# Performance work log

Measured on AMD Instinct MI355X. Metric: run time of the kernel, lower is better.

The kernel has to match this reference:

```python
import jax, jax.numpy as jnp
import numpy as np

D = 128
N = 768
EPS = 1e-5

def _layernorm(x, w, b):
    m = jnp.mean(x, axis=-1, keepdims=True)
    v = jnp.mean(jnp.square(x - m), axis=-1, keepdims=True)
    return (x - m) * jax.lax.rsqrt(v + EPS) * w + b

def _linear(x, w, b):
    # torch Linear convention: w is [out, in]
    return jnp.einsum('...i,oi->...o', x, w) + b

def setup_inputs() -> dict:
    key = jax.random.key(0)
    ks = jax.random.split(key, 8)
    s = 1.0 / np.sqrt(D)
    d = {
        'pair': jax.random.normal(ks[0], (N, N, D), dtype=jnp.float32),
        'ln_in_w': jnp.ones((D,), jnp.float32), 'ln_in_b': jnp.zeros((D,), jnp.float32),
        'lp_w': jax.random.uniform(ks[1], (D, D), jnp.float32, -s, s), 'lp_b': jnp.zeros((D,), jnp.float32),
        'lg_w': jax.random.uniform(ks[2], (D, D), jnp.float32, -s, s), 'lg_b': jnp.zeros((D,), jnp.float32),
        'rp_w': jax.random.uniform(ks[3], (D, D), jnp.float32, -s, s), 'rp_b': jnp.zeros((D,), jnp.float32),
        'rg_w': jax.random.uniform(ks[4], (D, D), jnp.float32, -s, s), 'rg_b': jnp.zeros((D,), jnp.float32),
        'cn_w': jnp.ones((D,), jnp.float32), 'cn_b': jnp.zeros((D,), jnp.float32),
        'op_w': jax.random.uniform(ks[5], (D, D), jnp.float32, -s, s), 'op_b': jnp.zeros((D,), jnp.float32),
        'og_w': jax.random.uniform(ks[6], (D, D), jnp.float32, -s, s), 'og_b': jnp.zeros((D,), jnp.float32),
        'ln_out_w': jnp.ones((D,), jnp.float32), 'ln_out_b': jnp.zeros((D,), jnp.float32),
    }
    return d

def reference(pair, ln_in_w, ln_in_b, lp_w, lp_b, lg_w, lg_b, rp_w, rp_b, rg_w, rg_b,
              cn_w, cn_b, op_w, op_b, og_w, og_b, ln_out_w, ln_out_b):
    z = _layernorm(pair, ln_in_w, ln_in_b)
    left = jax.nn.sigmoid(_linear(z, lg_w, lg_b)) * _linear(z, lp_w, lp_b)
    right = jax.nn.sigmoid(_linear(z, rg_w, rg_b)) * _linear(z, rp_w, rp_b)
    # outgoing direction: pair(i,j) = sum_k left(i,k,d) * right(j,k,d)
    tri = jnp.einsum('ikd,jkd->ijd', left, right)
    tri = _layernorm(tri, cn_w, cn_b)
    tri = jax.nn.sigmoid(_linear(pair, og_w, og_b)) * _linear(tri, op_w, op_b)
    return _layernorm(pair + tri, ln_out_w, ln_out_b)
```

## Files before the change

kernel.cpp:

```cpp
#include <hip/hip_runtime.h>

#define N 768
#define D 128
#define NSQ (N*N)
#define EPS 1e-5f

typedef __bf16 bf16;
typedef __bf16 bf16x8 __attribute__((ext_vector_type(8)));
typedef float f32x4 __attribute__((ext_vector_type(4)));

__device__ __forceinline__ void gld16(const void* g, void* l) {
    __builtin_amdgcn_global_load_lds(
        (const __attribute__((address_space(1))) unsigned int*)g,
        (__attribute__((address_space(3))) unsigned int*)l, 16, 0, 0);
}

__global__ void k_convert_w(const float* __restrict__ lp, const float* __restrict__ lg,
                            const float* __restrict__ rp, const float* __restrict__ rg,
                            const float* __restrict__ op, const float* __restrict__ og,
                            bf16* __restrict__ dst) {
    const float* srcs[6] = {lp, lg, rp, rg, op, og};
    int m = blockIdx.y;
    int i = blockIdx.x * 256 + threadIdx.x;
    dst[m * 16384 + i] = (bf16)srcs[m][i];
}

__global__ __launch_bounds__(512, 2) void k_ln_gate2(
    const float* __restrict__ pair, const float* __restrict__ lnw, const float* __restrict__ lnb,
    const bf16* __restrict__ wbf,
    const float* __restrict__ lp_b, const float* __restrict__ lg_b,
    const float* __restrict__ rp_b, const float* __restrict__ rg_b,
    bf16* __restrict__ left_t, bf16* __restrict__ right_t)
{
    __shared__ bf16 zt[2][64 * 128];

    const int t = threadIdx.x;
    const int lane = t & 63, wid = t >> 6;
    const int side = wid >> 2, dq = wid & 3;
    const int lr = lane & 15, lh = lane >> 4;

    const bf16* wPsrc = wbf + (side ? 2 : 0) * 16384;
    const bf16* wGsrc = wbf + (side ? 3 : 1) * 16384;
    const float* bPp = side ? rp_b : lp_b;
    const float* bGp = side ? rg_b : lg_b;
    bf16* dst = side ? right_t : left_t;

    bf16x8 aP[4][2], aG[4][2];
    #pragma unroll
    for (int kk = 0; kk < 4; ++kk)
        #pragma unroll
        for (int m = 0; m < 2; ++m) {
            int rd = dq * 32 + m * 16 + lr;
            aP[kk][m] = *(const bf16x8*)(wPsrc + rd * 128 + (kk * 4 + lh) * 8);
            aG[kk][m] = *(const bf16x8*)(wGsrc + rd * 128 + (kk * 4 + lh) * 8);
        }

    const int r8 = t >> 3, q = t & 7;

    f32x4 lw0 = *(const f32x4*)(lnw + q * 16);
    f32x4 lw1 = *(const f32x4*)(lnw + q * 16 + 4);
    f32x4 lw2 = *(const f32x4*)(lnw + q * 16 + 8);
    f32x4 lw3 = *(const f32x4*)(lnw + q * 16 + 12);
    f32x4 lb0 = *(const f32x4*)(lnb + q * 16);
    f32x4 lb1 = *(const f32x4*)(lnb + q * 16 + 4);
    f32x4 lb2 = *(const f32x4*)(lnb + q * 16 + 8);
    f32x4 lb3 = *(const f32x4*)(lnb + q * 16 + 12);

    const int bid = blockIdx.x, gstride = gridDim.x;

    f32x4 p0, p1, p2, p3;
    {
        const float* prow = pair + (size_t)(bid * 64 + r8) * 128 + q * 16;
        p0 = *(const f32x4*)(prow);
        p1 = *(const f32x4*)(prow + 4);
        p2 = *(const f32x4*)(prow + 8);
        p3 = *(const f32x4*)(prow + 12);
    }

    int buf = 0;
    for (int tile = bid; tile < NSQ / 64; tile += gstride) {
        const int row0 = tile * 64;

        float x[16];
        #pragma unroll
        for (int e = 0; e < 4; ++e) {
            x[e] = p0[e]; x[4 + e] = p1[e]; x[8 + e] = p2[e]; x[12 + e] = p3[e];
        }
        float s1 = 0.f, s2 = 0.f;
        #pragma unroll
        for (int j = 0; j < 16; ++j) { s1 += x[j]; s2 += x[j] * x[j]; }
        s1 += __shfl_xor(s1, 1); s2 += __shfl_xor(s2, 1);
        s1 += __shfl_xor(s1, 2); s2 += __shfl_xor(s2, 2);
        s1 += __shfl_xor(s1, 4); s2 += __shfl_xor(s2, 4);
        float mean = s1 * (1.f / 128.f);
        float rstd = rsqrtf(s2 * (1.f / 128.f) - mean * mean + EPS);

        bf16x8 pk0, pk1;
        #pragma unroll
        for (int e = 0; e < 4; ++e) {
            pk0[e]     = (bf16)((x[e]      - mean) * rstd * lw0[e] + lb0[e]);
            pk0[4 + e] = (bf16)((x[4 + e]  - mean) * rstd * lw1[e] + lb1[e]);
            pk1[e]     = (bf16)((x[8 + e]  - mean) * rstd * lw2[e] + lb2[e]);
            pk1[4 + e] = (bf16)((x[12 + e] - mean) * rstd * lw3[e] + lb3[e]);
        }
        {
            char* zb = (char*)&zt[buf][0];
            *(bf16x8*)(zb + r8 * 256 + ((q * 2)     ^ (r8 & 7)) * 16) = pk0;
            *(bf16x8*)(zb + r8 * 256 + ((q * 2 + 1) ^ (r8 & 7)) * 16) = pk1;
        }
        __syncthreads();

        int nt = tile + gstride;
        if (nt < NSQ / 64) {
            const float* prow = pair + (size_t)(nt * 64 + r8) * 128 + q * 16;
            p0 = *(const f32x4*)(prow);
            p1 = *(const f32x4*)(prow + 4);
            p2 = *(const f32x4*)(prow + 8);
            p3 = *(const f32x4*)(prow + 12);
        }

        f32x4 accP[2][4] = {};
        f32x4 accG[2][4] = {};
        const char* zb = (const char*)&zt[buf][0];
        #pragma unroll
        for (int kk = 0; kk < 4; ++kk) {
            bf16x8 bz[4];
            #pragma unroll
            for (int n = 0; n < 4; ++n) {
                int rz = n * 16 + lr;
                bz[n] = *(const bf16x8*)(zb + rz * 256 + (((kk * 4 + lh)) ^ (rz & 7)) * 16);
            }
            #pragma unroll
            for (int m = 0; m < 2; ++m)
                #pragma unroll
                for (int n = 0; n < 4; ++n) {
                    accP[m][n] = __builtin_amdgcn_mfma_f32_16x16x32_bf16(aP[kk][m], bz[n], accP[m][n], 0, 0, 0);
                    accG[m][n] = __builtin_amdgcn_mfma_f32_16x16x32_bf16(aG[kk][m], bz[n], accG[m][n], 0, 0, 0);
                }
        }

        #pragma unroll
        for (int m = 0; m < 2; ++m) {
            f32x4 vbP = *(const f32x4*)(bPp + dq * 32 + m * 16 + lh * 4);
            f32x4 vbG = *(const f32x4*)(bGp + dq * 32 + m * 16 + lh * 4);
            #pragma unroll
            for (int reg = 0; reg < 4; ++reg) {
                int d = dq * 32 + m * 16 + lh * 4 + reg;
                #pragma unroll
                for (int n = 0; n < 4; ++n) {
                    float g = accG[m][n][reg] + vbG[reg];
                    float p = accP[m][n][reg] + vbP[reg];
                    float val = p * (1.f / (1.f + __expf(-g)));
                    dst[(size_t)d * NSQ + row0 + n * 16 + lr] = (bf16)val;
                }
            }
        }
        buf ^= 1;
        __syncthreads();
    }
}

__global__ __launch_bounds__(256, 4) void k_tri(
    const bf16* __restrict__ left_t, const bf16* __restrict__ right_t, bf16* __restrict__ tri_t)
{
    __shared__ bf16 at[2][128 * 32];
    __shared__ bf16 bt[2][128 * 32];
    const int t = threadIdx.x;
    const int b = blockIdx.x;
    const int xcd = b & 7;
    const int s = b >> 3;
    const int d = xcd * 16 + s / 36;
    const int tile = s % 36;
    const int ti = tile / 6, tj = tile % 6;
    const bf16* A = left_t + (size_t)d * NSQ;
    const bf16* B = right_t + (size_t)d * NSQ;
    const int i0 = ti * 128, j0 = tj * 128;

    auto stage = [&](int buf, int kt) {
        int k0 = kt * 32;
        #pragma unroll
        for (int c = 0; c < 2; ++c) {
            int sl = c * 256 + t;
            int r = sl >> 2, cp = sl & 3, cl = cp ^ ((r >> 1) & 3);
            gld16(A + (size_t)(i0 + r) * 768 + k0 + cl * 8, (char*)at[buf] + sl * 16);
            gld16(B + (size_t)(j0 + r) * 768 + k0 + cl * 8, (char*)bt[buf] + sl * 16);
        }
    };

    const int lane = t & 63, wid = t >> 6;
    const int wr = wid >> 1, wc = wid & 1;
    const int lr = lane & 15, lh = lane >> 4;

    f32x4 acc[4][4] = {};

    stage(0, 0);
    __syncthreads();
    for (int kt = 0; kt < 24; ++kt) {
        if (kt < 23) stage((kt + 1) & 1, kt + 1);
        const bf16* ab = at[kt & 1];
        const bf16* bb = bt[kt & 1];
        bf16x8 af[4], bff[4];
        #pragma unroll
        for (int m = 0; m < 4; ++m) {
            int r = wr * 64 + m * 16 + lr;
            int phys = lh ^ ((r >> 1) & 3);
            af[m] = *(const bf16x8*)((const char*)ab + r * 64 + phys * 16);
        }
        #pragma unroll
        for (int n = 0; n < 4; ++n) {
            int r = wc * 64 + n * 16 + lr;
            int phys = lh ^ ((r >> 1) & 3);
            bff[n] = *(const bf16x8*)((const char*)bb + r * 64 + phys * 16);
        }
        #pragma unroll
        for (int m = 0; m < 4; ++m)
            #pragma unroll
            for (int n = 0; n < 4; ++n)
                acc[m][n] = __builtin_amdgcn_mfma_f32_16x16x32_bf16(af[m], bff[n], acc[m][n], 0, 0, 0);
        __syncthreads();
    }

    bf16* C = tri_t + (size_t)d * NSQ;
    #pragma unroll
    for (int m = 0; m < 4; ++m)
        #pragma unroll
        for (int n = 0; n < 4; ++n)
            #pragma unroll
            for (int reg = 0; reg < 4; ++reg) {
                int ri = i0 + wr * 64 + m * 16 + lh * 4 + reg;
                int cj = j0 + wc * 64 + n * 16 + lr;
                C[(size_t)ri * 768 + cj] = (bf16)acc[m][n][reg];
            }
}

__global__ __launch_bounds__(256, 2) void k_cln(
    const bf16* __restrict__ tri_t, const float* __restrict__ cnw, const float* __restrict__ cnb,
    bf16* __restrict__ tri_ln)
{
    __shared__ bf16 tile[256 * 128];
    __shared__ float mrs[256][2];
    const int t = threadIdx.x;
    const size_t ij = (size_t)blockIdx.x * 256 + t;
    float s1 = 0.f, s2 = 0.f;
    for (int dc = 0; dc < 16; ++dc) {
        bf16x8 pk;
        #pragma unroll
        for (int e = 0; e < 8; ++e) {
            int dd = dc * 8 + e;
            bf16 raw = tri_t[(size_t)dd * NSQ + ij];
            float v = (float)raw;
            s1 += v; s2 += v * v;
            pk[e] = raw;
        }
        *(bf16x8*)((char*)tile + t * 256 + (dc ^ (t & 7)) * 16) = pk;
    }
    float mean = s1 * (1.f / 128.f);
    float rstd = rsqrtf(s2 * (1.f / 128.f) - mean * mean + EPS);
    mrs[t][0] = mean; mrs[t][1] = rstd;
    __syncthreads();
    const size_t ij0 = (size_t)blockIdx.x * 256;
    #pragma unroll
    for (int c = 0; c < 16; ++c) {
        int sl = c * 256 + t;
        int rl = sl >> 4, cp = sl & 15, cl = cp ^ (rl & 7);
        bf16x8 raw = *(const bf16x8*)((const char*)tile + rl * 256 + cp * 16);
        float m = mrs[rl][0], r = mrs[rl][1];
        f32x4 w0 = *(const f32x4*)(cnw + cl * 8);
        f32x4 w1 = *(const f32x4*)(cnw + cl * 8 + 4);
        f32x4 b0 = *(const f32x4*)(cnb + cl * 8);
        f32x4 b1 = *(const f32x4*)(cnb + cl * 8 + 4);
        bf16x8 o;
        #pragma unroll
        for (int e = 0; e < 4; ++e) {
            o[e]     = (bf16)(((float)raw[e]     - m) * r * w0[e] + b0[e]);
            o[4 + e] = (bf16)(((float)raw[4 + e] - m) * r * w1[e] + b1[e]);
        }
        *(bf16x8*)(tri_ln + (ij0 + rl) * 128 + cl * 8) = o;
    }
}

__global__ __launch_bounds__(512, 2) void k_final2(
    const float* __restrict__ pair, const bf16* __restrict__ tri_ln,
    const bf16* __restrict__ wbf,
    const float* __restrict__ op_b, const float* __restrict__ og_b,
    const float* __restrict__ lnow, const float* __restrict__ lnob,
    float* __restrict__ out)
{
    __shared__ bf16 zt[64 * 128];
    __shared__ bf16 tt[2][64 * 128];
    __shared__ float ub[64 * 132];

    const int t = threadIdx.x;
    const int lane = t & 63, wid = t >> 6;
    const int dq = wid & 3, wh = wid >> 2;
    const int lr = lane & 15, lh = lane >> 4;

    const bf16* opsrc = wbf + 4 * 16384;
    const bf16* ogsrc = wbf + 5 * 16384;

    bf16x8 aOG[4][2], aOP[4][2];
    #pragma unroll
    for (int kk = 0; kk < 4; ++kk)
        #pragma unroll
        for (int m = 0; m < 2; ++m) {
            int rd = dq * 32 + m * 16 + lr;
            aOG[kk][m] = *(const bf16x8*)(ogsrc + rd * 128 + (kk * 4 + lh) * 8);
            aOP[kk][m] = *(const bf16x8*)(opsrc + rd * 128 + (kk * 4 + lh) * 8);
        }
    f32x4 vbOG[2], vbOP[2];
    #pragma unroll
    for (int m = 0; m < 2; ++m) {
        vbOG[m] = *(const f32x4*)(og_b + dq * 32 + m * 16 + lh * 4);
        vbOP[m] = *(const f32x4*)(op_b + dq * 32 + m * 16 + lh * 4);
    }

    const int r8 = t >> 3, q = t & 7;
    f32x4 lw0 = *(const f32x4*)(lnow + q * 16);
    f32x4 lw1 = *(const f32x4*)(lnow + q * 16 + 4);
    f32x4 lw2 = *(const f32x4*)(lnow + q * 16 + 8);
    f32x4 lw3 = *(const f32x4*)(lnow + q * 16 + 12);
    f32x4 lb0 = *(const f32x4*)(lnob + q * 16);
    f32x4 lb1 = *(const f32x4*)(lnob + q * 16 + 4);
    f32x4 lb2 = *(const f32x4*)(lnob + q * 16 + 8);
    f32x4 lb3 = *(const f32x4*)(lnob + q * 16 + 12);

    const int bid = blockIdx.x, gstride = gridDim.x;

    auto stage_tt = [&](int buf, int tile) {
        const int row0 = tile * 64;
        #pragma unroll
        for (int c = 0; c < 2; ++c) {
            int s = c * 512 + t;
            int r = s >> 4, cp = s & 15, cl = cp ^ (r & 7);
            gld16(tri_ln + (size_t)(row0 + r) * 128 + cl * 8, (char*)tt[buf] + s * 16);
        }
    };

    f32x4 pA0, pA1, pA2, pA3;
    {
        const float* prow = pair + (size_t)(bid * 64 + r8) * 128 + q * 16;
        pA0 = *(const f32x4*)(prow);
        pA1 = *(const f32x4*)(prow + 4);
        pA2 = *(const f32x4*)(prow + 8);
        pA3 = *(const f32x4*)(prow + 12);
    }
    stage_tt(0, bid);

    int buf = 0;
    for (int tile = bid; tile < NSQ / 64; tile += gstride) {
        const int row0 = tile * 64;

        {
            bf16x8 pk0, pk1;
            #pragma unroll
            for (int e = 0; e < 4; ++e) {
                pk0[e]     = (bf16)pA0[e];
                pk0[4 + e] = (bf16)pA1[e];
                pk1[e]     = (bf16)pA2[e];
                pk1[4 + e] = (bf16)pA3[e];
            }
            char* zb = (char*)zt;
            *(bf16x8*)(zb + r8 * 256 + ((q * 2)     ^ (r8 & 7)) * 16) = pk0;
            *(bf16x8*)(zb + r8 * 256 + ((q * 2 + 1) ^ (r8 & 7)) * 16) = pk1;
        }
        __syncthreads();

        const int nt = tile + gstride;
        if (nt < NSQ / 64) stage_tt(buf ^ 1, nt);

        f32x4 pB0 = pA0, pB1 = pA1, pB2 = pA2, pB3 = pA3;
        if (nt < NSQ / 64) {
            const float* prow = pair + (size_t)(nt * 64 + r8) * 128 + q * 16;
            pB0 = *(const f32x4*)(prow);
            pB1 = *(const f32x4*)(prow + 4);
            pB2 = *(const f32x4*)(prow + 8);
            pB3 = *(const f32x4*)(prow + 12);
        }

        f32x4 accOG[2][2] = {};
        f32x4 accOP[2][2] = {};
        const char* zb = (const char*)zt;
        const char* tb = (const char*)tt[buf];
        #pragma unroll
        for (int kk = 0; kk < 4; ++kk) {
            bf16x8 bzp[2], bzt[2];
            #pragma unroll
            for (int n = 0; n < 2; ++n) {
                int rz = wh * 32 + n * 16 + lr;
                int phys = (kk * 4 + lh) ^ (rz & 7);
                bzp[n] = *(const bf16x8*)(zb + rz * 256 + phys * 16);
                bzt[n] = *(const bf16x8*)(tb + rz * 256 + phys * 16);
            }
            #pragma unroll
            for (int m = 0; m < 2; ++m)
                #pragma unroll
                for (int n = 0; n < 2; ++n) {
                    accOG[m][n] = __builtin_amdgcn_mfma_f32_16x16x32_bf16(aOG[kk][m], bzp[n], accOG[m][n], 0, 0, 0);
                    accOP[m][n] = __builtin_amdgcn_mfma_f32_16x16x32_bf16(aOP[kk][m], bzt[n], accOP[m][n], 0, 0, 0);
                }
        }

        #pragma unroll
        for (int m = 0; m < 2; ++m)
            #pragma unroll
            for (int n = 0; n < 2; ++n) {
                int rr = wh * 32 + n * 16 + lr;
                f32x4 v;
                #pragma unroll
                for (int reg = 0; reg < 4; ++reg) {
                    float g = accOG[m][n][reg] + vbOG[m][reg];
                    float p = accOP[m][n][reg] + vbOP[m][reg];
                    v[reg] = p * (1.f / (1.f + __expf(-g)));
                }
                *(f32x4*)(ub + rr * 132 + dq * 32 + m * 16 + lh * 4) = v;
            }
        __syncthreads();

        {
            float x[16];
            const float* ur = ub + r8 * 132 + q * 16;
            f32x4 u0 = *(const f32x4*)(ur);
            f32x4 u1 = *(const f32x4*)(ur + 4);
            f32x4 u2 = *(const f32x4*)(ur + 8);
            f32x4 u3 = *(const f32x4*)(ur + 12);
            #pragma unroll
            for (int e = 0; e < 4; ++e) {
                x[e]      = pA0[e] + u0[e];
                x[4 + e]  = pA1[e] + u1[e];
                x[8 + e]  = pA2[e] + u2[e];
                x[12 + e] = pA3[e] + u3[e];
            }
            float s1 = 0.f, s2 = 0.f;
            #pragma unroll
            for (int j = 0; j < 16; ++j) { s1 += x[j]; s2 += x[j] * x[j]; }
            s1 += __shfl_xor(s1, 1); s2 += __shfl_xor(s2, 1);
            s1 += __shfl_xor(s1, 2); s2 += __shfl_xor(s2, 2);
            s1 += __shfl_xor(s1, 4); s2 += __shfl_xor(s2, 4);
            float mean = s1 * (1.f / 128.f);
            float rstd = rsqrtf(s2 * (1.f / 128.f) - mean * mean + EPS);
            float* orow = out + (size_t)(row0 + r8) * 128 + q * 16;
            f32x4 o0, o1, o2, o3;
            #pragma unroll
            for (int e = 0; e < 4; ++e) {
                o0[e] = (x[e]      - mean) * rstd * lw0[e] + lb0[e];
                o1[e] = (x[4 + e]  - mean) * rstd * lw1[e] + lb1[e];
                o2[e] = (x[8 + e]  - mean) * rstd * lw2[e] + lb2[e];
                o3[e] = (x[12 + e] - mean) * rstd * lw3[e] + lb3[e];
            }
            *(f32x4*)(orow)      = o0;
            *(f32x4*)(orow + 4)  = o1;
            *(f32x4*)(orow + 8)  = o2;
            *(f32x4*)(orow + 12) = o3;
        }

        pA0 = pB0; pA1 = pB1; pA2 = pB2; pA3 = pB3;
        buf ^= 1;
    }
}

extern "C" void kernel_launch(void* const* d_in, const int* in_sizes, int n_in,
                              void* d_out, int out_size, void* d_ws, size_t ws_size,
                              hipStream_t stream) {
    const float* pair    = (const float*)d_in[0];
    const float* ln_in_w = (const float*)d_in[1];
    const float* ln_in_b = (const float*)d_in[2];
    const float* lp_w    = (const float*)d_in[3];
    const float* lp_b    = (const float*)d_in[4];
    const float* lg_w    = (const float*)d_in[5];
    const float* lg_b    = (const float*)d_in[6];
    const float* rp_w    = (const float*)d_in[7];
    const float* rp_b    = (const float*)d_in[8];
    const float* rg_w    = (const float*)d_in[9];
    const float* rg_b    = (const float*)d_in[10];
    const float* cn_w    = (const float*)d_in[11];
    const float* cn_b    = (const float*)d_in[12];
    const float* op_w    = (const float*)d_in[13];
    const float* op_b    = (const float*)d_in[14];
    const float* og_w    = (const float*)d_in[15];
    const float* og_b    = (const float*)d_in[16];
    const float* ln_out_w = (const float*)d_in[17];
    const float* ln_out_b = (const float*)d_in[18];

    const size_t HALF = (size_t)128 * NSQ * 2;
    char* ws = (char*)d_ws;
    bf16* wbf     = (bf16*)ws;
    bf16* right_t = (bf16*)(ws + 196608);
    bf16* tri_ln  = right_t;
    bf16* left_t  = (bf16*)d_out;
    bf16* tri_t   = (bf16*)((char*)d_out + HALF);

    k_convert_w<<<dim3(64, 6), 256, 0, stream>>>(lp_w, lg_w, rp_w, rg_w, op_w, og_w, wbf);
    k_ln_gate2<<<dim3(512), 512, 0, stream>>>(pair, ln_in_w, ln_in_b, wbf,
                                              lp_b, lg_b, rp_b, rg_b, left_t, right_t);
    k_tri<<<dim3(4608), 256, 0, stream>>>(left_t, right_t, tri_t);
    k_cln<<<dim3(NSQ / 256), 256, 0, stream>>>(tri_t, cn_w, cn_b, tri_ln);
    k_final2<<<dim3(512), 512, 0, stream>>>(pair, tri_ln, wbf, op_b, og_b,
                                            ln_out_w, ln_out_b, (float*)d_out);
}
```

Measured before the change: 595.3 us.

## Swap MFMA operands for vectorized bf16x4 stores and shrink final staging to bf16

Swaps the A/B operands of the MFMA calls in the gate and triangle kernels so each lane holds four consecutive output columns, then writes them as packed bf16x4 stores instead of scattered scalar bf16 stores. Bias loads are hoisted out of the loop. The final kernel stages the gated update in bf16 instead of fp32 shared memory, cutting LDS use, and both fused kernels raise their occupancy hint from 2 to 4 waves per EU. The bf16 staging adds rounding error before the residual add, and the higher occupancy hint may cause register spills.

```diff
diff --git a/kernel.cpp b/kernel.cpp
--- a/kernel.cpp
+++ b/kernel.cpp
@@ -6,6 +6,7 @@
 #define EPS 1e-5f
 
 typedef __bf16 bf16;
+typedef __bf16 bf16x4 __attribute__((ext_vector_type(4)));
 typedef __bf16 bf16x8 __attribute__((ext_vector_type(8)));
 typedef float f32x4 __attribute__((ext_vector_type(4)));
 
@@ -25,7 +26,7 @@
     dst[m * 16384 + i] = (bf16)srcs[m][i];
 }
 
-__global__ __launch_bounds__(512, 2) void k_ln_gate2(
+__global__ __launch_bounds__(512, 4) void k_ln_gate2(
     const float* __restrict__ pair, const float* __restrict__ lnw, const float* __restrict__ lnb,
     const bf16* __restrict__ wbf,
     const float* __restrict__ lp_b, const float* __restrict__ lg_b,
@@ -54,6 +55,12 @@
             aP[kk][m] = *(const bf16x8*)(wPsrc + rd * 128 + (kk * 4 + lh) * 8);
             aG[kk][m] = *(const bf16x8*)(wGsrc + rd * 128 + (kk * 4 + lh) * 8);
         }
+    float bP[2], bG[2];
+    #pragma unroll
+    for (int m = 0; m < 2; ++m) {
+        bP[m] = bPp[dq * 32 + m * 16 + lr];
+        bG[m] = bGp[dq * 32 + m * 16 + lr];
+    }
 
     const int r8 = t >> 3, q = t & 7;
 
@@ -134,25 +141,25 @@
             for (int m = 0; m < 2; ++m)
                 #pragma unroll
                 for (int n = 0; n < 4; ++n) {
-                    accP[m][n] = __builtin_amdgcn_mfma_f32_16x16x32_bf16(aP[kk][m], bz[n], accP[m][n], 0, 0, 0);
-                    accG[m][n] = __builtin_amdgcn_mfma_f32_16x16x32_bf16(aG[kk][m], bz[n], accG[m][n], 0, 0, 0);
+                    accP[m][n] = __builtin_amdgcn_mfma_f32_16x16x32_bf16(bz[n], aP[kk][m], accP[m][n], 0, 0, 0);
+                    accG[m][n] = __builtin_amdgcn_mfma_f32_16x16x32_bf16(bz[n], aG[kk][m], accG[m][n], 0, 0, 0);
                 }
         }
 
         #pragma unroll
         for (int m = 0; m < 2; ++m) {
-            f32x4 vbP = *(const f32x4*)(bPp + dq * 32 + m * 16 + lh * 4);
-            f32x4 vbG = *(const f32x4*)(bGp + dq * 32 + m * 16 + lh * 4);
-            #pragma unroll
-            for (int reg = 0; reg < 4; ++reg) {
-                int d = dq * 32 + m * 16 + lh * 4 + reg;
+            const int d = dq * 32 + m * 16 + lr;
+            bf16* drow = dst + (size_t)d * NSQ + row0 + lh * 4;
+            #pragma unroll
+            for (int n = 0; n < 4; ++n) {
+                bf16x4 pk;
                 #pragma unroll
-                for (int n = 0; n < 4; ++n) {
-                    float g = accG[m][n][reg] + vbG[reg];
-                    float p = accP[m][n][reg] + vbP[reg];
-                    float val = p * (1.f / (1.f + __expf(-g)));
-                    dst[(size_t)d * NSQ + row0 + n * 16 + lr] = (bf16)val;
+                for (int reg = 0; reg < 4; ++reg) {
+                    float g = accG[m][n][reg] + bG[m];
+                    float p = accP[m][n][reg] + bP[m];
+                    pk[reg] = (bf16)(p * (1.f / (1.f + __expf(-g))));
                 }
+                *(bf16x4*)(drow + n * 16) = pk;
             }
         }
         buf ^= 1;
@@ -216,21 +223,24 @@
         for (int m = 0; m < 4; ++m)
             #pragma unroll
             for (int n = 0; n < 4; ++n)
-                acc[m][n] = __builtin_amdgcn_mfma_f32_16x16x32_bf16(af[m], bff[n], acc[m][n], 0, 0, 0);
+                acc[m][n] = __builtin_amdgcn_mfma_f32_16x16x32_bf16(bff[n], af[m], acc[m][n], 0, 0, 0);
         __syncthreads();
     }
 
     bf16* C = tri_t + (size_t)d * NSQ;
     #pragma unroll
-    for (int m = 0; m < 4; ++m)
-        #pragma unroll
-        for (int n = 0; n < 4; ++n)
-            #pragma unroll
-            for (int reg = 0; reg < 4; ++reg) {
-                int ri = i0 + wr * 64 + m * 16 + lh * 4 + reg;
-                int cj = j0 + wc * 64 + n * 16 + lr;
-                C[(size_t)ri * 768 + cj] = (bf16)acc[m][n][reg];
-            }
+    for (int m = 0; m < 4; ++m) {
+        const int ri = i0 + wr * 64 + m * 16 + lr;
+        bf16* crow = C + (size_t)ri * 768 + j0 + wc * 64 + lh * 4;
+        #pragma unroll
+        for (int n = 0; n < 4; ++n) {
+            bf16x4 pk;
+            #pragma unroll
+            for (int reg = 0; reg < 4; ++reg)
+                pk[reg] = (bf16)acc[m][n][reg];
+            *(bf16x4*)(crow + n * 16) = pk;
+        }
+    }
 }
 
 __global__ __launch_bounds__(256, 2) void k_cln(
@@ -279,7 +289,7 @@
     }
 }
 
-__global__ __launch_bounds__(512, 2) void k_final2(
+__global__ __launch_bounds__(512, 4) void k_final2(
     const float* __restrict__ pair, const bf16* __restrict__ tri_ln,
     const bf16* __restrict__ wbf,
     const float* __restrict__ op_b, const float* __restrict__ og_b,
@@ -288,7 +298,7 @@
 {
     __shared__ bf16 zt[64 * 128];
     __shared__ bf16 tt[2][64 * 128];
-    __shared__ float ub[64 * 132];
+    __shared__ bf16 ub[64 * 136];
 
     const int t = threadIdx.x;
     const int lane = t & 63, wid = t >> 6;
@@ -405,30 +415,28 @@
             #pragma unroll
             for (int n = 0; n < 2; ++n) {
                 int rr = wh * 32 + n * 16 + lr;
-                f32x4 v;
+                bf16x4 v;
                 #pragma unroll
                 for (int reg = 0; reg < 4; ++reg) {
                     float g = accOG[m][n][reg] + vbOG[m][reg];
                     float p = accOP[m][n][reg] + vbOP[m][reg];
-                    v[reg] = p * (1.f / (1.f + __expf(-g)));
+                    v[reg] = (bf16)(p * (1.f / (1.f + __expf(-g))));
                 }
-                *(f32x4*)(ub + rr * 132 + dq * 32 + m * 16 + lh * 4) = v;
+                *(bf16x4*)(ub + rr * 136 + dq * 32 + m * 16 + lh * 4) = v;
             }
         __syncthreads();
 
         {
             float x[16];
-            const float* ur = ub + r8 * 132 + q * 16;
-            f32x4 u0 = *(const f32x4*)(ur);
-            f32x4 u1 = *(const f32x4*)(ur + 4);
-            f32x4 u2 = *(const f32x4*)(ur + 8);
-            f32x4 u3 = *(const f32x4*)(ur + 12);
+            const bf16* ur = ub + r8 * 136 + q * 16;
+            bf16x8 u0 = *(const bf16x8*)(ur);
+            bf16x8 u1 = *(const bf16x8*)(ur + 8);
             #pragma unroll
             for (int e = 0; e < 4; ++e) {
-                x[e]      = pA0[e] + u0[e];
-                x[4 + e]  = pA1[e] + u1[e];
-                x[8 + e]  = pA2[e] + u2[e];
-                x[12 + e] = pA3[e] + u3[e];
+                x[e]      = pA0[e] + (float)u0[e];
+                x[4 + e]  = pA1[e] + (float)u0[4 + e];
+                x[8 + e]  = pA2[e] + (float)u1[e];
+                x[12 + e] = pA3[e] + (float)u1[4 + e];
             }
             float s1 = 0.f, s2 = 0.f;
             #pragma unroll
```

New measurement: 1.234 ms. +107.2%, slower.
